# Kernel optimization log

Measured on AMD Instinct MI355X. Metric: run time of the kernel, lower is better.

The kernel has to match this reference:

```python
import jax, jax.numpy as jnp
import numpy as np


def setup_inputs() -> dict:
    key = jax.random.key(0)
    k1, k2, k3, k4 = jax.random.split(key, 4)
    B, L, D_IN, D_OUT, E = 512, 50, 768, 300, 8
    x = jax.random.normal(k1, (B, L, D_IN), dtype=jnp.float32)
    w_gate = jax.random.normal(k2, (D_IN, E), dtype=jnp.float32) * 0.02
    expert_w = jax.random.normal(k3, (E, D_OUT, D_IN), dtype=jnp.float32) * 0.02
    expert_bias = jax.random.normal(k4, (E, L, D_IN), dtype=jnp.float32) * 0.02
    return {"x": x, "w_gate": w_gate, "expert_w": expert_w, "expert_bias": expert_bias}


def reference(x, w_gate, expert_w, expert_bias):
    # Gating (eval mode: noisy gating disabled) -> softmax over experts
    gates = jax.nn.softmax(x @ w_gate, axis=-1)  # [B, L, E]
    # DTRLayer: lin(x - bias) = x @ W^T - bias @ W^T (linearity avoids [B,L,E,D_in] intermediate)
    xw = jnp.einsum('bli,eoi->bleo', x, expert_w)           # [B, L, E, O]
    bw = jnp.einsum('eli,eoi->leo', expert_bias, expert_w)  # [L, E, O]
    expert_out = xw - bw[None]                              # [B, L, E, O]
    # Gate-weighted sum over experts
    return jnp.einsum('ble,bleo->blo', gates, expert_out)   # [B, L, O]
```

## Files before the change

kernel.cpp:

```cpp
#include <hip/hip_runtime.h>
#include <hip/hip_bf16.h>

#define BATCH   512
#define LSEQ    50
#define DIN     768
#define DOUT    300
#define NEXP    8
#define NTOK    (BATCH * LSEQ)

typedef __bf16 bf16_t;
typedef __attribute__((ext_vector_type(8))) __bf16 bf16x8;
typedef __attribute__((ext_vector_type(4))) float f32x4;

#define GLDS16(g, l) __builtin_amdgcn_global_load_lds( \
    (__attribute__((address_space(1))) void*)(g), \
    (__attribute__((address_space(3))) void*)(l), 16, 0, 0)

static __device__ __forceinline__ unsigned short f2bf(float f) {
    unsigned u = __float_as_uint(f);
    u = (u + 0x7fff + ((u >> 16) & 1)) >> 16;
    return (unsigned short)u;
}

__global__ __launch_bounds__(256) void cvt_gates_kernel(
    const float* __restrict__ x, const float* __restrict__ wg,
    unsigned short* __restrict__ xb, float* __restrict__ gates)
{
    __shared__ float wgT[NEXP][DIN + 4];

    const int tid  = threadIdx.x;
    #pragma unroll
    for (int r = 0; r < 6; ++r) {
        int j = tid + 256 * r;
        float4 v = ((const float4*)wg)[j];
        int i  = j >> 1;
        int e0 = (j & 1) * 4;
        wgT[e0 + 0][i] = v.x;
        wgT[e0 + 1][i] = v.y;
        wgT[e0 + 2][i] = v.z;
        wgT[e0 + 3][i] = v.w;
    }
    __syncthreads();

    int t    = blockIdx.x * 4 + (tid >> 6);
    int lane = tid & 63;
    const float4* xr = (const float4*)(x + (size_t)t * DIN);
    ushort4* xo = (ushort4*)(xb + (size_t)t * DIN);

    float acc[NEXP];
    #pragma unroll
    for (int e = 0; e < NEXP; e++) acc[e] = 0.0f;

    #pragma unroll
    for (int k = 0; k < 3; ++k) {
        int i4 = lane + 64 * k;
        float4 v = xr[i4];
        ushort4 u;
        u.x = f2bf(v.x); u.y = f2bf(v.y); u.z = f2bf(v.z); u.w = f2bf(v.w);
        xo[i4] = u;
        #pragma unroll
        for (int e = 0; e < NEXP; ++e) {
            float4 wv = *(const float4*)&wgT[e][4 * i4];
            acc[e] += v.x * wv.x + v.y * wv.y + v.z * wv.z + v.w * wv.w;
        }
    }
    #pragma unroll
    for (int e = 0; e < NEXP; e++) {
        #pragma unroll
        for (int m = 32; m > 0; m >>= 1) acc[e] += __shfl_xor(acc[e], m, 64);
    }
    float mx = acc[0];
    #pragma unroll
    for (int e = 1; e < NEXP; e++) mx = fmaxf(mx, acc[e]);
    float ex[NEXP]; float s = 0.0f;
    #pragma unroll
    for (int e = 0; e < NEXP; e++) { ex[e] = __expf(acc[e] - mx); s += ex[e]; }
    float inv = 1.0f / s;
    if (lane == 0) {
        #pragma unroll
        for (int e = 0; e < NEXP; e++) gates[(size_t)t * NEXP + e] = ex[e] * inv;
    }
}

__global__ __launch_bounds__(256) void bw_cvtw_kernel(
    const float* __restrict__ bias, const float* __restrict__ W,
    float* __restrict__ bw, unsigned short* __restrict__ wb)
{
    int wid  = blockIdx.x * 4 + (threadIdx.x >> 6);
    int lane = threadIdx.x & 63;
    int half = wid & 1;
    int eo   = wid >> 1;
    int e = eo / DOUT, o = eo % DOUT;

    const float4* wr = (const float4*)(W + ((size_t)e * DOUT + o) * DIN);
    float4 w4[3];
    #pragma unroll
    for (int k = 0; k < 3; ++k) w4[k] = wr[lane + 64 * k];

    if (half == 0) {
        ushort4* wo = (ushort4*)(wb + ((size_t)e * DOUT + o) * DIN);
        #pragma unroll
        for (int k = 0; k < 3; ++k) {
            ushort4 u;
            u.x = f2bf(w4[k].x); u.y = f2bf(w4[k].y);
            u.z = f2bf(w4[k].z); u.w = f2bf(w4[k].w);
            wo[lane + 64 * k] = u;
        }
    }

    int l0 = 25 * half;
    for (int l = l0; l < l0 + 25; ++l) {
        const float4* br = (const float4*)(bias + ((size_t)e * LSEQ + l) * DIN);
        float acc = 0.0f;
        #pragma unroll
        for (int k = 0; k < 3; ++k) {
            float4 b = br[lane + 64 * k];
            acc += b.x * w4[k].x + b.y * w4[k].y + b.z * w4[k].z + b.w * w4[k].w;
        }
        #pragma unroll
        for (int m = 32; m > 0; m >>= 1) acc += __shfl_xor(acc, m, 64);
        if (lane == 0) bw[((size_t)l * NEXP + e) * DOUT + o] = acc;
    }
}

#define GTM 256
#define GTO 16
#define GBK 32
#define GKIT (DIN / GBK)

__global__ __launch_bounds__(256, 2) void moe_mfma_kernel(
    const bf16_t* __restrict__ xb, const bf16_t* __restrict__ wb,
    const float* __restrict__ gates, const float* __restrict__ bw,
    float* __restrict__ out)
{
    __shared__ f32x4 ldsv[1536];
    char* Xs = (char*)ldsv;
    char* Ws = (char*)ldsv + 16384;

    const int tid  = threadIdx.x;
    const int w    = tid >> 6;
    const int lane = tid & 63;
    const int o0   = blockIdx.x * GTO;
    const int t0   = blockIdx.y * GTM;

    const int srow4 = lane >> 2;
    const int c16   = 16 * ((lane & 3) ^ ((lane >> 4) & 3));

    const char* xg[4];
    #pragma unroll
    for (int j = 0; j < 4; ++j)
        xg[j] = (const char*)xb + (size_t)(t0 + 64 * w + 16 * j + srow4) * (DIN * 2) + c16;
    char* xl = Xs + 4096 * w;

    const char* wg[2];
    #pragma unroll
    for (int j = 0; j < 2; ++j) {
        int n = 32 * w + 16 * j + srow4;
        int e = n >> 4;
        int o = o0 + (n & 15); if (o >= DOUT) o = DOUT - 1;
        wg[j] = (const char*)wb + (size_t)(e * DOUT + o) * (DIN * 2) + c16;
    }
    char* wl = Ws + 2048 * w;

    const int m = lane & 15, q = lane >> 4;
    const int sw = 16 * (q ^ ((m >> 2) & 3));
    int aoff[4], boff[8];
    #pragma unroll
    for (int rf = 0; rf < 4; ++rf) aoff[rf] = 64 * (64 * w + 16 * rf + m) + sw;
    #pragma unroll
    for (int cf = 0; cf < 8; ++cf) boff[cf] = 64 * (16 * cf + m) + sw;

    f32x4 acc[4][8] = {};

    for (int it = 0; it < GKIT; ++it) {
        #pragma unroll
        for (int j = 0; j < 4; ++j) GLDS16(xg[j], xl + 1024 * j);
        #pragma unroll
        for (int j = 0; j < 2; ++j) GLDS16(wg[j], wl + 1024 * j);
        #pragma unroll
        for (int j = 0; j < 4; ++j) xg[j] += 64;
        #pragma unroll
        for (int j = 0; j < 2; ++j) wg[j] += 64;
        __syncthreads();

        bf16x8 a[4];
        #pragma unroll
        for (int rf = 0; rf < 4; ++rf) a[rf] = *(const bf16x8*)(Xs + aoff[rf]);
        #pragma unroll
        for (int cf = 0; cf < 8; ++cf) {
            bf16x8 b = *(const bf16x8*)(Ws + boff[cf]);
            #pragma unroll
            for (int rf = 0; rf < 4; ++rf)
                acc[rf][cf] = __builtin_amdgcn_mfma_f32_16x16x32_bf16(a[rf], b, acc[rf][cf], 0, 0, 0);
        }
        __syncthreads();
    }

    const int o = o0 + m;
    if (o < DOUT) {
        #pragma unroll
        for (int rf = 0; rf < 4; ++rf) {
            #pragma unroll
            for (int r = 0; r < 4; ++r) {
                int t = t0 + 64 * w + 16 * rf + 4 * q + r;
                int l = t % LSEQ;
                float4 g0 = *(const float4*)(gates + (size_t)t * NEXP);
                float4 g1 = *(const float4*)(gates + (size_t)t * NEXP + 4);
                const float* bp = bw + (size_t)l * NEXP * DOUT + o;
                float s = 0.0f;
                s += g0.x * (acc[rf][0][r] - bp[0 * DOUT]);
                s += g0.y * (acc[rf][1][r] - bp[1 * DOUT]);
                s += g0.z * (acc[rf][2][r] - bp[2 * DOUT]);
                s += g0.w * (acc[rf][3][r] - bp[3 * DOUT]);
                s += g1.x * (acc[rf][4][r] - bp[4 * DOUT]);
                s += g1.y * (acc[rf][5][r] - bp[5 * DOUT]);
                s += g1.z * (acc[rf][6][r] - bp[6 * DOUT]);
                s += g1.w * (acc[rf][7][r] - bp[7 * DOUT]);
                out[(size_t)t * DOUT + o] = s;
            }
        }
    }
}

__global__ __launch_bounds__(256) void gates_kernel(
    const float* __restrict__ x, const float* __restrict__ wg,
    float* __restrict__ gates)
{
    int t    = blockIdx.x * 4 + (threadIdx.x >> 6);
    int lane = threadIdx.x & 63;
    const float* xr = x + (size_t)t * DIN;
    float acc[NEXP];
    #pragma unroll
    for (int e = 0; e < NEXP; e++) acc[e] = 0.0f;
    for (int i = lane; i < DIN; i += 64) {
        float xv = xr[i];
        const float* wr = wg + (size_t)i * NEXP;
        #pragma unroll
        for (int e = 0; e < NEXP; e++) acc[e] += xv * wr[e];
    }
    #pragma unroll
    for (int e = 0; e < NEXP; e++) {
        #pragma unroll
        for (int m = 32; m > 0; m >>= 1) acc[e] += __shfl_xor(acc[e], m, 64);
    }
    float mx = acc[0];
    #pragma unroll
    for (int e = 1; e < NEXP; e++) mx = fmaxf(mx, acc[e]);
    float ex[NEXP]; float s = 0.0f;
    #pragma unroll
    for (int e = 0; e < NEXP; e++) { ex[e] = __expf(acc[e] - mx); s += ex[e]; }
    float inv = 1.0f / s;
    if (lane == 0) {
        #pragma unroll
        for (int e = 0; e < NEXP; e++) gates[(size_t)t * NEXP + e] = ex[e] * inv;
    }
}

__global__ __launch_bounds__(256) void bw_kernel(
    const float* __restrict__ bias, const float* __restrict__ W,
    float* __restrict__ bw)
{
    int wave = blockIdx.x * 4 + (threadIdx.x >> 6);
    int lane = threadIdx.x & 63;
    int l   = wave / (NEXP * DOUT);
    int rem = wave % (NEXP * DOUT);
    int e   = rem / DOUT;
    int o   = rem % DOUT;
    const float4* br = (const float4*)(bias + ((size_t)e * LSEQ + l) * DIN);
    const float4* wr = (const float4*)(W    + ((size_t)e * DOUT + o) * DIN);
    float acc = 0.0f;
    #pragma unroll
    for (int k = 0; k < 3; ++k) {
        int i4 = lane + 64 * k;
        float4 b = br[i4], w = wr[i4];
        acc += b.x * w.x + b.y * w.y + b.z * w.z + b.w * w.w;
    }
    #pragma unroll
    for (int m = 32; m > 0; m >>= 1) acc += __shfl_xor(acc, m, 64);
    if (lane == 0) bw[((size_t)l * NEXP + e) * DOUT + o] = acc;
}

#define TM  64
#define TO  16
#define KT  32
#define KTP 36

__global__ __launch_bounds__(256) void moe_main_kernel(
    const float* __restrict__ x, const float* __restrict__ W,
    const float* __restrict__ gates, const float* __restrict__ bw,
    float* __restrict__ out)
{
    __shared__ float Xs[TM][KTP];
    __shared__ float Wls[128][KTP];
    const int tid = threadIdx.x;
    const int t0 = blockIdx.x * TM;
    const int o0 = blockIdx.y * TO;
    const int cg = tid & 15;
    const int tg = tid >> 4;
    const int lrow = tid >> 3;
    const int lk4  = (tid & 7) * 4;
    float acc[4][NEXP];
    #pragma unroll
    for (int i = 0; i < 4; i++)
        #pragma unroll
        for (int j = 0; j < NEXP; j++) acc[i][j] = 0.0f;
    for (int k0 = 0; k0 < DIN; k0 += KT) {
        #pragma unroll
        for (int r = 0; r < 2; r++) {
            int row = lrow + 32 * r;
            float4 v = *(const float4*)&x[((size_t)(t0 + row)) * DIN + k0 + lk4];
            *(float4*)&Xs[row][lk4] = v;
        }
        #pragma unroll
        for (int r = 0; r < 4; r++) {
            int nl = lrow + 32 * r;
            int e  = nl >> 4;
            int o  = o0 + (nl & 15);
            float4 v;
            if (o < DOUT)
                v = *(const float4*)&W[((size_t)e * DOUT + o) * DIN + k0 + lk4];
            else
                v = make_float4(0.f, 0.f, 0.f, 0.f);
            *(float4*)&Wls[nl][lk4] = v;
        }
        __syncthreads();
        #pragma unroll
        for (int k4 = 0; k4 < KT; k4 += 4) {
            float4 xa[4], wb4[NEXP];
            #pragma unroll
            for (int i = 0; i < 4; i++)
                xa[i] = *(const float4*)&Xs[tg + 16 * i][k4];
            #pragma unroll
            for (int j = 0; j < NEXP; j++)
                wb4[j] = *(const float4*)&Wls[cg + 16 * j][k4];
            #pragma unroll
            for (int i = 0; i < 4; i++)
                #pragma unroll
                for (int j = 0; j < NEXP; j++) {
                    acc[i][j] += xa[i].x * wb4[j].x;
                    acc[i][j] += xa[i].y * wb4[j].y;
                    acc[i][j] += xa[i].z * wb4[j].z;
                    acc[i][j] += xa[i].w * wb4[j].w;
                }
        }
        __syncthreads();
    }
    const int o = o0 + cg;
    if (o < DOUT) {
        #pragma unroll
        for (int i = 0; i < 4; i++) {
            int t = t0 + tg + 16 * i;
            int l = t % LSEQ;
            float s = 0.0f;
            #pragma unroll
            for (int j = 0; j < NEXP; j++) {
                float g = gates[(size_t)t * NEXP + j];
                s += g * (acc[i][j] - bw[((size_t)l * NEXP + j) * DOUT + o]);
            }
            out[(size_t)t * DOUT + o] = s;
        }
    }
}

extern "C" void kernel_launch(void* const* d_in, const int* in_sizes, int n_in,
                              void* d_out, int out_size, void* d_ws, size_t ws_size,
                              hipStream_t stream) {
    const float* x     = (const float*)d_in[0];
    const float* wgate = (const float*)d_in[1];
    const float* ew    = (const float*)d_in[2];
    const float* ebias = (const float*)d_in[3];
    float* out = (float*)d_out;

    const size_t n_gates = (size_t)NTOK * NEXP;
    const size_t n_bw    = (size_t)LSEQ * NEXP * DOUT;
    const size_t n_x     = (size_t)NTOK * DIN;
    const size_t n_w     = (size_t)NEXP * DOUT * DIN;

    float* gates = (float*)d_ws;
    float* bw    = gates + n_gates;
    bf16_t* xb   = (bf16_t*)(bw + n_bw);
    bf16_t* wbuf = xb + n_x;

    const size_t need = (n_gates + n_bw) * 4 + (n_x + n_w) * 2;

    if (ws_size >= need) {
        cvt_gates_kernel<<<NTOK / 4, 256, 0, stream>>>(
            x, wgate, (unsigned short*)xb, gates);
        bw_cvtw_kernel<<<(2 * NEXP * DOUT) / 4, 256, 0, stream>>>(
            ebias, ew, bw, (unsigned short*)wbuf);
        dim3 grid((DOUT + GTO - 1) / GTO, NTOK / GTM);
        moe_mfma_kernel<<<grid, 256, 0, stream>>>(xb, wbuf, gates, bw, out);
    } else {
        gates_kernel<<<NTOK / 4, 256, 0, stream>>>(x, wgate, gates);
        bw_kernel<<<(LSEQ * NEXP * DOUT) / 4, 256, 0, stream>>>(ebias, ew, bw);
        dim3 grid(NTOK / TM, (DOUT + TO - 1) / TO);
        moe_main_kernel<<<grid, 256, 0, stream>>>(x, ew, gates, bw, out);
    }
}
```

Before: 277.0 us.

## Merge prep kernels into one launch and remap GEMM blocks for XCD-local reuse

The gate/convert kernel and the bias-projection/weight-convert kernel become one launch, with the job chosen by block index. This removes a kernel launch and lets the two independent prep jobs run at the same time. The MFMA kernel now uses a 1D grid whose block index is remapped so that blocks sharing bid&7 (likely one XCD each) handle a contiguous group of row tiles across all output tiles. This aims to improve L2 reuse of the x tiles, at the cost of some idle early-exit blocks (8*13*19 launched vs 100*19 needed).

After: 270.4 us. 2.4% less time.

```diff
diff --git a/kernel.cpp b/kernel.cpp
--- a/kernel.cpp
+++ b/kernel.cpp
@@ -22,104 +22,105 @@
     return (unsigned short)u;
 }
 
-__global__ __launch_bounds__(256) void cvt_gates_kernel(
+#define PREP_GATE_BLOCKS (NTOK / 4)
+#define PREP_BW_BLOCKS   ((2 * NEXP * DOUT) / 4)
+
+__global__ __launch_bounds__(256) void prep_kernel(
     const float* __restrict__ x, const float* __restrict__ wg,
-    unsigned short* __restrict__ xb, float* __restrict__ gates)
-{
-    __shared__ float wgT[NEXP][DIN + 4];
-
-    const int tid  = threadIdx.x;
-    #pragma unroll
-    for (int r = 0; r < 6; ++r) {
-        int j = tid + 256 * r;
-        float4 v = ((const float4*)wg)[j];
-        int i  = j >> 1;
-        int e0 = (j & 1) * 4;
-        wgT[e0 + 0][i] = v.x;
-        wgT[e0 + 1][i] = v.y;
-        wgT[e0 + 2][i] = v.z;
-        wgT[e0 + 3][i] = v.w;
-    }
-    __syncthreads();
-
-    int t    = blockIdx.x * 4 + (tid >> 6);
-    int lane = tid & 63;
-    const float4* xr = (const float4*)(x + (size_t)t * DIN);
-    ushort4* xo = (ushort4*)(xb + (size_t)t * DIN);
-
-    float acc[NEXP];
-    #pragma unroll
-    for (int e = 0; e < NEXP; e++) acc[e] = 0.0f;
-
-    #pragma unroll
-    for (int k = 0; k < 3; ++k) {
-        int i4 = lane + 64 * k;
-        float4 v = xr[i4];
-        ushort4 u;
-        u.x = f2bf(v.x); u.y = f2bf(v.y); u.z = f2bf(v.z); u.w = f2bf(v.w);
-        xo[i4] = u;
-        #pragma unroll
-        for (int e = 0; e < NEXP; ++e) {
-            float4 wv = *(const float4*)&wgT[e][4 * i4];
-            acc[e] += v.x * wv.x + v.y * wv.y + v.z * wv.z + v.w * wv.w;
-        }
-    }
-    #pragma unroll
-    for (int e = 0; e < NEXP; e++) {
-        #pragma unroll
-        for (int m = 32; m > 0; m >>= 1) acc[e] += __shfl_xor(acc[e], m, 64);
-    }
-    float mx = acc[0];
-    #pragma unroll
-    for (int e = 1; e < NEXP; e++) mx = fmaxf(mx, acc[e]);
-    float ex[NEXP]; float s = 0.0f;
-    #pragma unroll
-    for (int e = 0; e < NEXP; e++) { ex[e] = __expf(acc[e] - mx); s += ex[e]; }
-    float inv = 1.0f / s;
-    if (lane == 0) {
-        #pragma unroll
-        for (int e = 0; e < NEXP; e++) gates[(size_t)t * NEXP + e] = ex[e] * inv;
-    }
-}
-
-__global__ __launch_bounds__(256) void bw_cvtw_kernel(
     const float* __restrict__ bias, const float* __restrict__ W,
+    unsigned short* __restrict__ xb, float* __restrict__ gates,
     float* __restrict__ bw, unsigned short* __restrict__ wb)
 {
-    int wid  = blockIdx.x * 4 + (threadIdx.x >> 6);
-    int lane = threadIdx.x & 63;
-    int half = wid & 1;
-    int eo   = wid >> 1;
-    int e = eo / DOUT, o = eo % DOUT;
-
-    const float4* wr = (const float4*)(W + ((size_t)e * DOUT + o) * DIN);
-    float4 w4[3];
-    #pragma unroll
-    for (int k = 0; k < 3; ++k) w4[k] = wr[lane + 64 * k];
-
-    if (half == 0) {
-        ushort4* wo = (ushort4*)(wb + ((size_t)e * DOUT + o) * DIN);
+    const int tid  = threadIdx.x;
+    const int lane = tid & 63;
+
+    if (blockIdx.x < PREP_GATE_BLOCKS) {
+        __shared__ float wgT[NEXP][DIN + 4];
+        #pragma unroll
+        for (int r = 0; r < 6; ++r) {
+            int j = tid + 256 * r;
+            float4 v = ((const float4*)wg)[j];
+            int i  = j >> 1;
+            int e0 = (j & 1) * 4;
+            wgT[e0 + 0][i] = v.x;
+            wgT[e0 + 1][i] = v.y;
+            wgT[e0 + 2][i] = v.z;
+            wgT[e0 + 3][i] = v.w;
+        }
+        __syncthreads();
+
+        int t = blockIdx.x * 4 + (tid >> 6);
+        const float4* xr = (const float4*)(x + (size_t)t * DIN);
+        ushort4* xo = (ushort4*)(xb + (size_t)t * DIN);
+
+        float acc[NEXP];
+        #pragma unroll
+        for (int e = 0; e < NEXP; e++) acc[e] = 0.0f;
+
         #pragma unroll
         for (int k = 0; k < 3; ++k) {
+            int i4 = lane + 64 * k;
+            float4 v = xr[i4];
             ushort4 u;
-            u.x = f2bf(w4[k].x); u.y = f2bf(w4[k].y);
-            u.z = f2bf(w4[k].z); u.w = f2bf(w4[k].w);
-            wo[lane + 64 * k] = u;
-        }
-    }
-
-    int l0 = 25 * half;
-    for (int l = l0; l < l0 + 25; ++l) {
-        const float4* br = (const float4*)(bias + ((size_t)e * LSEQ + l) * DIN);
-        float acc = 0.0f;
-        #pragma unroll
-        for (int k = 0; k < 3; ++k) {
-            float4 b = br[lane + 64 * k];
-            acc += b.x * w4[k].x + b.y * w4[k].y + b.z * w4[k].z + b.w * w4[k].w;
-        }
-        #pragma unroll
-        for (int m = 32; m > 0; m >>= 1) acc += __shfl_xor(acc, m, 64);
-        if (lane == 0) bw[((size_t)l * NEXP + e) * DOUT + o] = acc;
+            u.x = f2bf(v.x); u.y = f2bf(v.y); u.z = f2bf(v.z); u.w = f2bf(v.w);
+            xo[i4] = u;
+            #pragma unroll
+            for (int e = 0; e < NEXP; ++e) {
+                float4 wv = *(const float4*)&wgT[e][4 * i4];
+                acc[e] += v.x * wv.x + v.y * wv.y + v.z * wv.z + v.w * wv.w;
+            }
+        }
+        #pragma unroll
+        for (int e = 0; e < NEXP; e++) {
+            #pragma unroll
+            for (int m = 32; m > 0; m >>= 1) acc[e] += __shfl_xor(acc[e], m, 64);
+        }
+        float mx = acc[0];
+        #pragma unroll
+        for (int e = 1; e < NEXP; e++) mx = fmaxf(mx, acc[e]);
+        float ex[NEXP]; float s = 0.0f;
+        #pragma unroll
+        for (int e = 0; e < NEXP; e++) { ex[e] = __expf(acc[e] - mx); s += ex[e]; }
+        float inv = 1.0f / s;
+        if (lane == 0) {
+            #pragma unroll
+            for (int e = 0; e < NEXP; e++) gates[(size_t)t * NEXP + e] = ex[e] * inv;
+        }
+    } else {
+        int wid  = (blockIdx.x - PREP_GATE_BLOCKS) * 4 + (tid >> 6);
+        int half = wid & 1;
+        int eo   = wid >> 1;
+        int e = eo / DOUT, o = eo % DOUT;
+
+        const float4* wr = (const float4*)(W + ((size_t)e * DOUT + o) * DIN);
+        float4 w4[3];
+        #pragma unroll
+        for (int k = 0; k < 3; ++k) w4[k] = wr[lane + 64 * k];
+
+        if (half == 0) {
+            ushort4* wo = (ushort4*)(wb + ((size_t)e * DOUT + o) * DIN);
+            #pragma unroll
+            for (int k = 0; k < 3; ++k) {
+                ushort4 u;
+                u.x = f2bf(w4[k].x); u.y = f2bf(w4[k].y);
+                u.z = f2bf(w4[k].z); u.w = f2bf(w4[k].w);
+                wo[lane + 64 * k] = u;
+            }
+        }
+
+        int l0 = 25 * half;
+        for (int l = l0; l < l0 + 25; ++l) {
+            const float4* br = (const float4*)(bias + ((size_t)e * LSEQ + l) * DIN);
+            float acc = 0.0f;
+            #pragma unroll
+            for (int k = 0; k < 3; ++k) {
+                float4 b = br[lane + 64 * k];
+                acc += b.x * w4[k].x + b.y * w4[k].y + b.z * w4[k].z + b.w * w4[k].w;
+            }
+            #pragma unroll
+            for (int m = 32; m > 0; m >>= 1) acc += __shfl_xor(acc, m, 64);
+            if (lane == 0) bw[((size_t)l * NEXP + e) * DOUT + o] = acc;
+        }
     }
 }
 
@@ -127,12 +128,25 @@
 #define GTO 16
 #define GBK 32
 #define GKIT (DIN / GBK)
+#define NRT  (NTOK / GTM)
+#define NOT  19
+#define RPG  13
 
 __global__ __launch_bounds__(256, 2) void moe_mfma_kernel(
     const bf16_t* __restrict__ xb, const bf16_t* __restrict__ wb,
     const float* __restrict__ gates, const float* __restrict__ bw,
     float* __restrict__ out)
 {
+    const int bid  = blockIdx.x;
+    const int g    = bid & 7;
+    const int slot = bid >> 3;
+    const int r_in = slot / NOT;
+    const int o_t  = slot - NOT * r_in;
+    const int r_t  = g * RPG + r_in;
+    if (r_t >= NRT) return;
+    const int o0 = o_t * GTO;
+    const int t0 = r_t * GTM;
+
     __shared__ f32x4 ldsv[1536];
     char* Xs = (char*)ldsv;
     char* Ws = (char*)ldsv + 16384;
@@ -140,8 +154,6 @@
     const int tid  = threadIdx.x;
     const int w    = tid >> 6;
     const int lane = tid & 63;
-    const int o0   = blockIdx.x * GTO;
-    const int t0   = blockIdx.y * GTM;
 
     const int srow4 = lane >> 2;
     const int c16   = 16 * ((lane & 3) ^ ((lane >> 4) & 3));
@@ -384,12 +396,9 @@
     const size_t need = (n_gates + n_bw) * 4 + (n_x + n_w) * 2;
 
     if (ws_size >= need) {
-        cvt_gates_kernel<<<NTOK / 4, 256, 0, stream>>>(
-            x, wgate, (unsigned short*)xb, gates);
-        bw_cvtw_kernel<<<(2 * NEXP * DOUT) / 4, 256, 0, stream>>>(
-            ebias, ew, bw, (unsigned short*)wbuf);
-        dim3 grid((DOUT + GTO - 1) / GTO, NTOK / GTM);
-        moe_mfma_kernel<<<grid, 256, 0, stream>>>(xb, wbuf, gates, bw, out);
+        prep_kernel<<<PREP_GATE_BLOCKS + PREP_BW_BLOCKS, 256, 0, stream>>>(
+            x, wgate, ebias, ew, (unsigned short*)xb, gates, bw, (unsigned short*)wbuf);
+        moe_mfma_kernel<<<8 * RPG * NOT, 256, 0, stream>>>(xb, wbuf, gates, bw, out);
     } else {
         gates_kernel<<<NTOK / 4, 256, 0, stream>>>(x, wgate, gates);
         bw_kernel<<<(LSEQ * NEXP * DOUT) / 4, 256, 0, stream>>>(ebias, ew, bw);
```
